# Performance work log

Hardware: AMD Instinct MI355X
Metric: run time of the kernel (lower is better)

The kernel has to match this reference:

```python
import jax, jax.numpy as jnp
import numpy as np

B, S, D, H, KD, VD, HID, L, V, OUTN = 16, 512, 512, 8, 64, 64, 2048, 4, 32000, 128
EPS = 1e-5


def _layer_norm(x, g, b):
    m = jnp.mean(x, axis=-1, keepdims=True)
    v = jnp.mean(jnp.square(x - m), axis=-1, keepdims=True)
    return (x - m) * jax.lax.rsqrt(v + EPS) * g + b


def _pos_encoding(seq_len, d_model):
    pos = jnp.arange(seq_len, dtype=jnp.float32)[:, None]
    div = jnp.exp(jnp.arange(0, d_model, 2, dtype=jnp.float32) * (-np.log(10000.0) / d_model))
    pe = jnp.zeros((seq_len, d_model), dtype=jnp.float32)
    pe = pe.at[:, 0::2].set(jnp.sin(pos * div))
    pe = pe.at[:, 1::2].set(jnp.cos(pos * div))
    return pe


def setup_inputs() -> dict:
    key = jax.random.key(0)
    ks = jax.random.split(key, 32)
    s = 0.02
    n = jax.random.normal
    inp = {
        "enc_inputs": jax.random.randint(ks[0], (B, S), 0, V, dtype=jnp.int32),
        "emb": n(ks[1], (V, D), jnp.float32) * s,
        # stacked per-layer params, leading dim = L
        "Wq": n(ks[2], (L, D, H * KD), jnp.float32) * s,
        "bq": jnp.zeros((L, H * KD), jnp.float32),
        "Wk": n(ks[3], (L, D, H * KD), jnp.float32) * s,
        "bk": jnp.zeros((L, H * KD), jnp.float32),
        "Wv": n(ks[4], (L, D, H * VD), jnp.float32) * s,
        "bv": jnp.zeros((L, H * VD), jnp.float32),
        "Wo": n(ks[5], (L, H * VD, D), jnp.float32) * s,
        "bo": jnp.zeros((L, D), jnp.float32),
        "ln1_g": jnp.ones((L, D), jnp.float32),
        "ln1_b": jnp.zeros((L, D), jnp.float32),
        "W1": n(ks[6], (L, D, HID), jnp.float32) * s,   # conv1d k=1 == linear
        "b1": jnp.zeros((L, HID), jnp.float32),
        "W2": n(ks[7], (L, HID, D), jnp.float32) * s,
        "b2": jnp.zeros((L, D), jnp.float32),
        "ln2_g": jnp.ones((L, D), jnp.float32),
        "ln2_b": jnp.zeros((L, D), jnp.float32),
        # flatten head created inside torch forward: [S*D, 128]
        "Wf": n(ks[8], (S * D, OUTN), jnp.float32) * s,
        "bf": jnp.zeros((OUTN,), jnp.float32),
        "Wout": n(ks[9], (OUTN, 1), jnp.float32) * s,
        "bout": jnp.zeros((1,), jnp.float32),
    }
    return inp


def _encoder(enc_inputs, emb, Wq, bq, Wk, bk, Wv, bv, Wo, bo, ln1_g, ln1_b,
             W1, b1, W2, b2, ln2_g, ln2_b, Wf, bf, Wout, bout):
    x = emb[enc_inputs] + _pos_encoding(S, D)[None, :, :]          # [B,S,D]
    pad = (enc_inputs == 0)[:, None, None, :]                      # [B,1,1,S]
    scale = 1.0 / np.sqrt(D)                                       # note: sqrt(embed_dim), as in source
    for l in range(L):
        # multi-head attention
        q = (x @ Wq[l] + bq[l]).reshape(B, S, H, KD)
        k = (x @ Wk[l] + bk[l]).reshape(B, S, H, KD)
        v = (x @ Wv[l] + bv[l]).reshape(B, S, H, VD)
        scores = jnp.einsum('bqhd,bkhd->bhqk', q, k) * scale
        scores = jnp.where(pad, -1e9, scores)
        attn = jax.nn.softmax(scores, axis=-1)
        ctx = jnp.einsum('bhqk,bkhd->bqhd', attn, v).reshape(B, S, H * VD)
        x = _layer_norm(ctx @ Wo[l] + bo[l] + x, ln1_g[l], ln1_b[l])
        # position-wise FFN (conv1d kernel_size=1)
        h = jax.nn.relu(x @ W1[l] + b1[l])
        x = _layer_norm(h @ W2[l] + b2[l] + x, ln2_g[l], ln2_b[l])
    flat = x.reshape(B, S * D)
    features = flat @ Wf + bf                                      # [B,128]
    y_score = jax.nn.sigmoid(features @ Wout + bout)               # [B,1]
    y_pred = jnp.round(y_score)
    return y_score, y_pred, features


def reference(enc_inputs, emb, Wq, bq, Wk, bk, Wv, bv, Wo, bo, ln1_g, ln1_b,
              W1, b1, W2, b2, ln2_g, ln2_b, Wf, bf, Wout, bout):
    return _encoder(enc_inputs, emb, Wq, bq, Wk, bk, Wv, bv, Wo, bo, ln1_g, ln1_b,
                    W1, b1, W2, b2, ln2_g, ln2_b, Wf, bf, Wout, bout)
```

## Files before the change

### kernel.cpp

```cpp
#include <hip/hip_runtime.h>
#include <hip/hip_bf16.h>
#include <math.h>

typedef unsigned short ushort_t;
typedef __attribute__((ext_vector_type(8))) short bf16x8;
typedef __attribute__((ext_vector_type(4))) float f32x4;

#define SCALE_QK 0.04419417382415922f
#define PE_C 0.017988946039015986f

__device__ __forceinline__ void g2lds16(const void* g, void* l) {
    __builtin_amdgcn_global_load_lds(
        (const __attribute__((address_space(1))) unsigned int*)g,
        (__attribute__((address_space(3))) unsigned int*)l,
        16, 0, 0);
}
__device__ __forceinline__ ushort_t f2bs(float v) {
    __hip_bfloat16 h = __float2bfloat16(v);
    return *reinterpret_cast<ushort_t*>(&h);
}
__device__ __forceinline__ float bs2f(ushort_t v) {
    return __uint_as_float(((unsigned int)v) << 16);
}

template<int BM, int BN, bool RELU, bool VT, bool STATS>
__global__ __launch_bounds__(256) void gemm2(
    const ushort_t* __restrict__ A, const ushort_t* __restrict__ B,
    const float* __restrict__ bias, const ushort_t* __restrict__ resb,
    ushort_t* __restrict__ C, float2* __restrict__ part,
    ushort_t* __restrict__ vt, int K, int lda, int ldb, int ldc)
{
    constexpr int MI = BM / 32, NJ = BN / 32;
    __shared__ ushort_t As[BM * 64];
    __shared__ ushort_t Bs[BN * 64];

    const int t = threadIdx.x;
    const int lane = t & 63, w = t >> 6;
    const int l16 = lane & 15, quad = lane >> 4;
    const int r8 = lane >> 3;
    const int kg = ((lane & 7) ^ r8) << 3;
    const int wm = (w >> 1) * (BM / 2);
    const int wn = (w & 1) * (BN / 2);

    const int m0 = blockIdx.y * BM, n0 = blockIdx.x * BN;

    f32x4 acc[MI][NJ];
    #pragma unroll
    for (int i = 0; i < MI; i++)
        #pragma unroll
        for (int j = 0; j < NJ; j++)
            acc[i][j] = (f32x4){0.f, 0.f, 0.f, 0.f};

    for (int k0 = 0; k0 < K; k0 += 64) {
        #pragma unroll
        for (int ii = 0; ii < BM / 32; ii++) {
            int rbase = w * (BM / 4) + ii * 8;
            g2lds16(A + (size_t)(m0 + rbase + r8) * lda + k0 + kg, &As[rbase * 64]);
        }
        #pragma unroll
        for (int ii = 0; ii < BN / 32; ii++) {
            int rbase = w * (BN / 4) + ii * 8;
            g2lds16(B + (size_t)(n0 + rbase + r8) * ldb + k0 + kg, &Bs[rbase * 64]);
        }
        __syncthreads();

        #pragma unroll
        for (int tt = 0; tt < 2; tt++) {
            bf16x8 af[MI], bf[NJ];
            #pragma unroll
            for (int i = 0; i < MI; i++) {
                int row = wm + i * 16 + l16;
                af[i] = *(const bf16x8*)&As[row * 64 + ((((tt << 2) + quad) ^ (row & 7)) << 3)];
            }
            #pragma unroll
            for (int j = 0; j < NJ; j++) {
                int row = wn + j * 16 + l16;
                bf[j] = *(const bf16x8*)&Bs[row * 64 + ((((tt << 2) + quad) ^ (row & 7)) << 3)];
            }
            #pragma unroll
            for (int i = 0; i < MI; i++)
                #pragma unroll
                for (int j = 0; j < NJ; j++)
                    acc[i][j] = __builtin_amdgcn_mfma_f32_16x16x32_bf16(
                        af[i], bf[j], acc[i][j], 0, 0, 0);
        }
        __syncthreads();
    }

    if (VT && n0 >= 1024) {
        #pragma unroll
        for (int i = 0; i < MI; i++) {
            int mbase = m0 + wm + i * 16 + quad * 4;
            int b = mbase >> 9, s = mbase & 511;
            #pragma unroll
            for (int j = 0; j < NJ; j++) {
                int n = n0 + wn + j * 16 + l16;
                int hv = n - 1024;
                int h = hv >> 6, vd = hv & 63;
                float bv = bias[n];
                ushort4 pk;
                pk.x = f2bs(acc[i][j][0] + bv);
                pk.y = f2bs(acc[i][j][1] + bv);
                pk.z = f2bs(acc[i][j][2] + bv);
                pk.w = f2bs(acc[i][j][3] + bv);
                *(ushort4*)&vt[((size_t)((b << 3) + h)) * 32768 + (size_t)vd * 512 + s] = pk;
            }
        }
        return;
    }

    #pragma unroll
    for (int i = 0; i < MI; i++) {
        float rs[4] = {0.f, 0.f, 0.f, 0.f}, rq[4] = {0.f, 0.f, 0.f, 0.f};
        #pragma unroll
        for (int j = 0; j < NJ; j++) {
            int n = n0 + wn + j * 16 + l16;
            float bv = bias ? bias[n] : 0.f;
            #pragma unroll
            for (int r = 0; r < 4; r++) {
                int m = m0 + wm + i * 16 + quad * 4 + r;
                float v = acc[i][j][r] + bv;
                if (resb) v += bs2f(resb[(size_t)m * ldc + n]);
                if (RELU) v = fmaxf(v, 0.f);
                C[(size_t)m * ldc + n] = f2bs(v);
                if (STATS) { rs[r] += v; rq[r] += v * v; }
            }
        }
        if (STATS) {
            #pragma unroll
            for (int r = 0; r < 4; r++) {
                float s = rs[r], q = rq[r];
                #pragma unroll
                for (int off = 1; off < 16; off <<= 1) {
                    s += __shfl_xor(s, off);
                    q += __shfl_xor(q, off);
                }
                if (l16 == 0) {
                    int m = m0 + wm + i * 16 + quad * 4 + r;
                    part[(size_t)m * 16 + blockIdx.x * 2 + (w & 1)] = make_float2(s, q);
                }
            }
        }
    }
}

template<bool RELU, bool VT>
__global__ __launch_bounds__(512, 2) void gemm8(
    const ushort_t* __restrict__ A, const ushort_t* __restrict__ B,
    const float* __restrict__ bias, ushort_t* __restrict__ C,
    ushort_t* __restrict__ vt, int K, int lda, int ldb, int ldc)
{
    __shared__ ushort_t As[2][256 * 64];
    __shared__ ushort_t Bs[2][256 * 64];

    const int t = threadIdx.x;
    const int lane = t & 63, w = t >> 6;
    const int l16 = lane & 15, quad = lane >> 4;
    const int r8 = lane >> 3;
    const int kg = ((lane & 7) ^ r8) << 3;
    const int wm = (w >> 2) * 128;
    const int wn = (w & 3) * 64;
    const int m0 = blockIdx.y * 256, n0 = blockIdx.x * 256;
    const int NT = K >> 6;

    f32x4 acc[8][4];
    #pragma unroll
    for (int i = 0; i < 8; i++)
        #pragma unroll
        for (int j = 0; j < 4; j++)
            acc[i][j] = (f32x4){0.f, 0.f, 0.f, 0.f};

    auto STAGE8 = [&](int kt, int bb) {
        int k0 = kt << 6;
        #pragma unroll
        for (int ii = 0; ii < 4; ii++) {
            int rbase = w * 32 + ii * 8;
            g2lds16(A + (size_t)(m0 + rbase + r8) * lda + k0 + kg,
                    &As[bb][rbase * 64]);
            g2lds16(B + (size_t)(n0 + rbase + r8) * ldb + k0 + kg,
                    &Bs[bb][rbase * 64]);
        }
    };

    STAGE8(0, 0);
    STAGE8(1, 1);

    for (int kt = 0; kt < NT; kt++) {
        const int bb = kt & 1;
        if (kt < NT - 1)
            asm volatile("s_waitcnt vmcnt(8)" ::: "memory");
        else
            asm volatile("s_waitcnt vmcnt(0)" ::: "memory");
        __builtin_amdgcn_s_barrier();
        asm volatile("" ::: "memory");

        #pragma unroll
        for (int tt = 0; tt < 2; tt++) {
            bf16x8 af[8], bf[4];
            #pragma unroll
            for (int i = 0; i < 8; i++) {
                int row = wm + i * 16 + l16;
                af[i] = *(const bf16x8*)&As[bb][row * 64 + ((((tt << 2) + quad) ^ (row & 7)) << 3)];
            }
            #pragma unroll
            for (int j = 0; j < 4; j++) {
                int row = wn + j * 16 + l16;
                bf[j] = *(const bf16x8*)&Bs[bb][row * 64 + ((((tt << 2) + quad) ^ (row & 7)) << 3)];
            }
            #pragma unroll
            for (int i = 0; i < 8; i++)
                #pragma unroll
                for (int j = 0; j < 4; j++)
                    acc[i][j] = __builtin_amdgcn_mfma_f32_16x16x32_bf16(
                        af[i], bf[j], acc[i][j], 0, 0, 0);
        }

        asm volatile("" ::: "memory");
        __builtin_amdgcn_s_barrier();
        asm volatile("" ::: "memory");
        if (kt + 2 < NT)
            STAGE8(kt + 2, bb);
    }

    if (VT && n0 >= 1024) {
        #pragma unroll
        for (int i = 0; i < 8; i++) {
            int mbase = m0 + wm + i * 16 + quad * 4;
            int b = mbase >> 9, s = mbase & 511;
            #pragma unroll
            for (int j = 0; j < 4; j++) {
                int n = n0 + wn + j * 16 + l16;
                int hv = n - 1024;
                int h = hv >> 6, vd = hv & 63;
                float bv = bias[n];
                ushort4 pk;
                pk.x = f2bs(acc[i][j][0] + bv);
                pk.y = f2bs(acc[i][j][1] + bv);
                pk.z = f2bs(acc[i][j][2] + bv);
                pk.w = f2bs(acc[i][j][3] + bv);
                *(ushort4*)&vt[((size_t)((b << 3) + h)) * 32768 + (size_t)vd * 512 + s] = pk;
            }
        }
        return;
    }

    #pragma unroll
    for (int i = 0; i < 8; i++)
        #pragma unroll
        for (int j = 0; j < 4; j++) {
            int n = n0 + wn + j * 16 + l16;
            float bv = bias[n];
            #pragma unroll
            for (int r = 0; r < 4; r++) {
                int m = m0 + wm + i * 16 + quad * 4 + r;
                float v = acc[i][j][r] + bv;
                if (RELU) v = fmaxf(v, 0.f);
                C[(size_t)m * ldc + n] = f2bs(v);
            }
        }
}

__global__ __launch_bounds__(256) void flash_attn(
    ushort_t* __restrict__ QKV, const ushort_t* __restrict__ Vt,
    const int* __restrict__ tok)
{
    __shared__ ushort_t Qs[128 * 64];
    __shared__ ushort_t Ks[128 * 64];
    __shared__ ushort_t Vts[64 * 128];
    __shared__ ushort_t Ps[128 * 128];

    const int bh = blockIdx.y;
    const int b = bh >> 3, h = bh & 7;
    const int q0 = blockIdx.x * 128;
    const int t = threadIdx.x;
    const int lane = t & 63, w = t >> 6;
    const int l16 = lane & 15, quad = lane >> 4;
    const int wm = w * 32;
    const size_t rowbase = (size_t)b * 512;

    {
        int r8 = lane >> 3;
        int kg = (lane & 7) ^ r8;
        #pragma unroll
        for (int ii = 0; ii < 4; ii++) {
            int rb = w * 32 + ii * 8;
            g2lds16(QKV + (rowbase + q0 + rb + r8) * 1536 + h * 64 + kg * 8,
                    &Qs[rb * 64]);
        }
    }

    f32x4 accO[2][4];
    #pragma unroll
    for (int i = 0; i < 2; i++)
        #pragma unroll
        for (int jv = 0; jv < 4; jv++)
            accO[i][jv] = (f32x4){0.f, 0.f, 0.f, 0.f};
    float lrow[2][4];
    #pragma unroll
    for (int i = 0; i < 2; i++)
        #pragma unroll
        for (int r = 0; r < 4; r++) lrow[i][r] = 0.f;

    for (int kc = 0; kc < 4; kc++) {
        __syncthreads();
        {
            int r8 = lane >> 3;
            int kg = (lane & 7) ^ r8;
            #pragma unroll
            for (int ii = 0; ii < 4; ii++) {
                int rb = w * 32 + ii * 8;
                g2lds16(QKV + (rowbase + kc * 128 + rb + r8) * 1536 + 512 + h * 64 + kg * 8,
                        &Ks[rb * 64]);
            }
        }
        {
            int v4 = lane >> 4;
            #pragma unroll
            for (int ii = 0; ii < 4; ii++) {
                int vb = w * 16 + ii * 4;
                int vd = vb + v4;
                int kg = (lane & 15) ^ (vd & 15);
                g2lds16(Vt + (size_t)bh * 32768 + (size_t)vd * 512 + kc * 128 + kg * 8,
                        &Vts[vb * 128]);
            }
        }
        float maskv[8];
        #pragma unroll
        for (int j = 0; j < 8; j++)
            maskv[j] = (tok[b * 512 + kc * 128 + j * 16 + l16] == 0) ? -1e9f : 0.f;

        __syncthreads();

        f32x4 sacc[2][8];
        #pragma unroll
        for (int i = 0; i < 2; i++)
            #pragma unroll
            for (int j = 0; j < 8; j++)
                sacc[i][j] = (f32x4){0.f, 0.f, 0.f, 0.f};
        #pragma unroll
        for (int tt = 0; tt < 2; tt++) {
            bf16x8 aq[2], bk8[8];
            #pragma unroll
            for (int i = 0; i < 2; i++) {
                int row = wm + i * 16 + l16;
                aq[i] = *(const bf16x8*)&Qs[row * 64 + (((tt << 2) + quad) ^ (row & 7)) * 8];
            }
            #pragma unroll
            for (int j = 0; j < 8; j++) {
                int row = j * 16 + l16;
                bk8[j] = *(const bf16x8*)&Ks[row * 64 + (((tt << 2) + quad) ^ (row & 7)) * 8];
            }
            #pragma unroll
            for (int i = 0; i < 2; i++)
                #pragma unroll
                for (int j = 0; j < 8; j++)
                    sacc[i][j] = __builtin_amdgcn_mfma_f32_16x16x32_bf16(
                        aq[i], bk8[j], sacc[i][j], 0, 0, 0);
        }

        #pragma unroll
        for (int i = 0; i < 2; i++)
            #pragma unroll
            for (int j = 0; j < 8; j++)
                #pragma unroll
                for (int r = 0; r < 4; r++) {
                    float p = __expf(fmaf(sacc[i][j][r], SCALE_QK, maskv[j]));
                    sacc[i][j][r] = p;
                    lrow[i][r] += p;
                }

        #pragma unroll
        for (int i = 0; i < 2; i++)
            #pragma unroll
            for (int j = 0; j < 8; j++) {
                int col = j * 16 + l16;
                int colc = col >> 3, csub = col & 7;
                #pragma unroll
                for (int r = 0; r < 4; r++) {
                    int row = wm + i * 16 + quad * 4 + r;
                    Ps[row * 128 + ((colc ^ (row & 15)) << 3) + csub] = f2bs(sacc[i][j][r]);
                }
            }

        #pragma unroll
        for (int tt = 0; tt < 4; tt++) {
            bf16x8 ap[2], bv8[4];
            #pragma unroll
            for (int i = 0; i < 2; i++) {
                int row = wm + i * 16 + l16;
                ap[i] = *(const bf16x8*)&Ps[row * 128 + ((((tt << 2) + quad)) ^ (row & 15)) * 8];
            }
            #pragma unroll
            for (int jv = 0; jv < 4; jv++) {
                int vd = jv * 16 + l16;
                bv8[jv] = *(const bf16x8*)&Vts[vd * 128 + (((tt << 2) + quad) ^ (vd & 15)) * 8];
            }
            #pragma unroll
            for (int i = 0; i < 2; i++)
                #pragma unroll
                for (int jv = 0; jv < 4; jv++)
                    accO[i][jv] = __builtin_amdgcn_mfma_f32_16x16x32_bf16(
                        ap[i], bv8[jv], accO[i][jv], 0, 0, 0);
        }
    }

    #pragma unroll
    for (int i = 0; i < 2; i++)
        #pragma unroll
        for (int r = 0; r < 4; r++) {
            float s = lrow[i][r];
            #pragma unroll
            for (int off = 1; off < 16; off <<= 1)
                s += __shfl_xor(s, off);
            float inv = 1.f / s;
            int row = q0 + wm + i * 16 + quad * 4 + r;
            #pragma unroll
            for (int jv = 0; jv < 4; jv++) {
                int vd = jv * 16 + l16;
                QKV[(rowbase + row) * 1536 + h * 64 + vd] = f2bs(accO[i][jv][r] * inv);
            }
        }
}

__global__ __launch_bounds__(256) void transpose_cvt(
    const float* __restrict__ in, __hip_bfloat16* __restrict__ out,
    int R, int Cc, long long inz, long long outz)
{
    in  += blockIdx.z * inz;
    out += blockIdx.z * outz;
    __shared__ float tile[32][33];
    int c0 = blockIdx.x * 32, r0 = blockIdx.y * 32;
    int tx = threadIdx.x & 31, ty = threadIdx.x >> 5;
    #pragma unroll
    for (int i = 0; i < 4; i++)
        tile[ty + i * 8][tx] = in[(size_t)(r0 + ty + i * 8) * Cc + c0 + tx];
    __syncthreads();
    #pragma unroll
    for (int i = 0; i < 4; i++)
        out[(size_t)(c0 + ty + i * 8) * R + r0 + tx] =
            __float2bfloat16(tile[tx][ty + i * 8]);
}

__global__ __launch_bounds__(256) void concat_bias(const float* __restrict__ bq,
                                                   const float* __restrict__ bk,
                                                   const float* __restrict__ bv,
                                                   float* __restrict__ bqkv) {
    int idx = blockIdx.x * 256 + threadIdx.x;
    if (idx >= 4 * 1536) return;
    int l = idx / 1536, n = idx - l * 1536;
    float v = (n < 512) ? bq[l * 512 + n]
            : (n < 1024) ? bk[l * 512 + n - 512]
                         : bv[l * 512 + n - 1024];
    bqkv[idx] = v;
}

__global__ __launch_bounds__(256) void embed_pe_b(const int* __restrict__ tok,
                                                  const float* __restrict__ emb,
                                                  __hip_bfloat16* __restrict__ xb) {
    int idx = blockIdx.x * 256 + threadIdx.x;
    int d  = idx & 511;
    int bs = idx >> 9;
    int s  = bs & 511;
    int t  = tok[bs];
    float freq  = expf(-(float)(d & ~1) * PE_C);
    float angle = (float)s * freq;
    float pe    = (d & 1) ? cosf(angle) : sinf(angle);
    xb[idx] = __float2bfloat16(emb[(size_t)t * 512 + d] + pe);
}

__global__ __launch_bounds__(256) void ln_stats(const ushort_t* __restrict__ Cpre,
                                                const float2* __restrict__ part,
                                                const float* __restrict__ g,
                                                const float* __restrict__ b,
                                                ushort_t* __restrict__ Xb) {
    long long row = blockIdx.x;
    int t = threadIdx.x;
    float s = 0.f, q = 0.f;
    if (t < 16) {
        float2 p = part[row * 16 + t];
        s = p.x; q = p.y;
    }
    #pragma unroll
    for (int off = 1; off < 16; off <<= 1) {
        s += __shfl_xor(s, off);
        q += __shfl_xor(q, off);
    }
    __shared__ float mv[2];
    if (t == 0) {
        float mean = s * (1.f / 512.f);
        float var = q * (1.f / 512.f) - mean * mean;
        mv[0] = mean;
        mv[1] = rsqrtf(var + 1e-5f);
    }
    __syncthreads();
    float mean = mv[0], r = mv[1];
    int c = t * 2;
    ushort2 u = *(const ushort2*)&Cpre[row * 512 + c];
    ushort2 o;
    o.x = f2bs((bs2f(u.x) - mean) * r * g[c]     + b[c]);
    o.y = f2bs((bs2f(u.y) - mean) * r * g[c + 1] + b[c + 1]);
    *(ushort2*)&Xb[row * 512 + c] = o;
}

__global__ __launch_bounds__(256) void feat_partial(const ushort_t* __restrict__ Xb,
                                                    const float* __restrict__ Wf,
                                                    float* __restrict__ FbP) {
    int slice = blockIdx.x;
    int k0 = slice * 512;
    __shared__ float Xs[16][512];
    int t = threadIdx.x;
    for (int i = t; i < 2048; i += 256) {
        int b = i >> 7, c4 = (i & 127) * 4;
        ushort4 u = *(const ushort4*)&Xb[(size_t)b * 262144 + k0 + c4];
        Xs[b][c4 + 0] = bs2f(u.x);
        Xs[b][c4 + 1] = bs2f(u.y);
        Xs[b][c4 + 2] = bs2f(u.z);
        Xs[b][c4 + 3] = bs2f(u.w);
    }
    __syncthreads();
    int n4 = (t & 31) * 4;
    int kh = t >> 5;
    float4 acc[16];
    #pragma unroll
    for (int b = 0; b < 16; b++) acc[b] = (float4){0.f, 0.f, 0.f, 0.f};
    for (int kk4 = 0; kk4 < 16; kk4++) {
        int kb = kh * 64 + kk4 * 4;
        float4 w0 = *(const float4*)&Wf[(size_t)(k0 + kb + 0) * 128 + n4];
        float4 w1 = *(const float4*)&Wf[(size_t)(k0 + kb + 1) * 128 + n4];
        float4 w2 = *(const float4*)&Wf[(size_t)(k0 + kb + 2) * 128 + n4];
        float4 w3 = *(const float4*)&Wf[(size_t)(k0 + kb + 3) * 128 + n4];
        #pragma unroll
        for (int b = 0; b < 16; b++) {
            float4 xq = *(const float4*)&Xs[b][kb];
            acc[b].x += xq.x * w0.x + xq.y * w1.x + xq.z * w2.x + xq.w * w3.x;
            acc[b].y += xq.x * w0.y + xq.y * w1.y + xq.z * w2.y + xq.w * w3.y;
            acc[b].z += xq.x * w0.z + xq.y * w1.z + xq.z * w2.z + xq.w * w3.z;
            acc[b].w += xq.x * w0.w + xq.y * w1.w + xq.z * w2.w + xq.w * w3.w;
        }
    }
    float* dst = FbP + ((size_t)slice * 8 + kh) * 2048;
    #pragma unroll
    for (int b = 0; b < 16; b++)
        *(float4*)&dst[b * 128 + n4] = acc[b];
}

__global__ __launch_bounds__(256) void feat_reduce(const float* __restrict__ FbP,
                                                   float* __restrict__ Fb) {
    int idx = blockIdx.x * 256 + threadIdx.x;
    int j0 = blockIdx.y * 128;
    float s = 0.f;
    for (int j = 0; j < 128; j++) s += FbP[(size_t)(j0 + j) * 2048 + idx];
    atomicAdd(&Fb[idx], s);
}

__global__ __launch_bounds__(256) void head_kernel(const float* __restrict__ feat,
                                                   const float* __restrict__ bfv,
                                                   const float* __restrict__ Wo2,
                                                   const float* __restrict__ bo2,
                                                   float* __restrict__ out) {
    __shared__ float f[2048];
    int t = threadIdx.x;
    for (int i = t; i < 2048; i += 256) {
        float v = feat[i] + bfv[i & 127];
        f[i] = v;
        out[32 + i] = v;
    }
    __syncthreads();
    if (t < 16) {
        float zv = bo2[0];
        for (int n = 0; n < 128; n++) zv = fmaf(f[t * 128 + n], Wo2[n], zv);
        float ys = 1.f / (1.f + expf(-zv));
        out[t] = ys;
        out[16 + t] = rintf(ys);
    }
}

extern "C" void kernel_launch(void* const* d_in, const int* in_sizes, int n_in,
                              void* d_out, int out_size, void* d_ws, size_t ws_size,
                              hipStream_t stream) {
    const int*   enc  = (const int*)  d_in[0];
    const float* emb  = (const float*)d_in[1];
    const float* Wq   = (const float*)d_in[2];
    const float* bq   = (const float*)d_in[3];
    const float* Wk   = (const float*)d_in[4];
    const float* bk   = (const float*)d_in[5];
    const float* Wv   = (const float*)d_in[6];
    const float* bv   = (const float*)d_in[7];
    const float* Wo   = (const float*)d_in[8];
    const float* bo   = (const float*)d_in[9];
    const float* g1   = (const float*)d_in[10];
    const float* be1  = (const float*)d_in[11];
    const float* W1   = (const float*)d_in[12];
    const float* b1f  = (const float*)d_in[13];
    const float* W2   = (const float*)d_in[14];
    const float* b2f  = (const float*)d_in[15];
    const float* g2   = (const float*)d_in[16];
    const float* be2  = (const float*)d_in[17];
    const float* Wf   = (const float*)d_in[18];
    const float* bf   = (const float*)d_in[19];
    const float* Wout = (const float*)d_in[20];
    const float* bout = (const float*)d_in[21];
    float* out = (float*)d_out;

    char* ws = (char*)d_ws;
    ushort_t* Cpre = (ushort_t*) (ws + 0);
    ushort_t* Xb   = (ushort_t*) (ws + 16777216);
    ushort_t* QKV  = (ushort_t*) (ws + 25165824);
    ushort_t* Vt   = (ushort_t*) (ws + 50331648);
    ushort_t* S    = (ushort_t*) (ws + 58720256);
    ushort_t* WqkvT= (ushort_t*) (ws + 92274688);
    ushort_t* WoT  = (ushort_t*) (ws + 98566144);
    ushort_t* W1T  = (ushort_t*) (ws + 100663296);
    ushort_t* W2T  = (ushort_t*) (ws + 109051904);
    float*    bqkv = (float*)    (ws + 117440512);
    float*    Fb   = (float*)    (ws + 117465088);
    float2*   part = (float2*)   (ws + 117473280);
    float*    FbP  = (float*)    (ws + 25165824);

    typedef __hip_bfloat16 bf16;

    transpose_cvt<<<dim3(16, 16, 4), 256, 0, stream>>>(Wq, (bf16*)WqkvT,            512, 512,  262144, 786432);
    transpose_cvt<<<dim3(16, 16, 4), 256, 0, stream>>>(Wk, (bf16*)(WqkvT + 262144), 512, 512,  262144, 786432);
    transpose_cvt<<<dim3(16, 16, 4), 256, 0, stream>>>(Wv, (bf16*)(WqkvT + 524288), 512, 512,  262144, 786432);
    transpose_cvt<<<dim3(16, 16, 4), 256, 0, stream>>>(Wo, (bf16*)WoT,              512, 512,  262144, 262144);
    transpose_cvt<<<dim3(64, 16, 4), 256, 0, stream>>>(W1, (bf16*)W1T,              512, 2048, 1048576, 1048576);
    transpose_cvt<<<dim3(16, 64, 4), 256, 0, stream>>>(W2, (bf16*)W2T,              2048, 512, 1048576, 1048576);
    concat_bias<<<24, 256, 0, stream>>>(bq, bk, bv, bqkv);

    embed_pe_b<<<16384, 256, 0, stream>>>(enc, emb, (bf16*)Xb);

    for (int l = 0; l < 4; l++) {
        gemm8<false, true><<<dim3(6, 32), 512, 0, stream>>>(
            Xb, WqkvT + (size_t)l * 786432, bqkv + l * 1536,
            QKV, Vt, 512, 512, 512, 1536);

        flash_attn<<<dim3(4, 128), 256, 0, stream>>>(QKV, Vt, enc);

        gemm2<128, 64, false, false, true><<<dim3(8, 64), 256, 0, stream>>>(
            QKV, WoT + (size_t)l * 262144, bo + l * 512, Xb,
            Cpre, part, nullptr, 512, 1536, 512, 512);
        ln_stats<<<8192, 256, 0, stream>>>(Cpre, part, g1 + l * 512, be1 + l * 512, Xb);

        gemm8<true, false><<<dim3(8, 32), 512, 0, stream>>>(
            Xb, W1T + (size_t)l * 1048576, b1f + l * 2048,
            S, nullptr, 512, 512, 512, 2048);
        gemm2<128, 64, false, false, true><<<dim3(8, 64), 256, 0, stream>>>(
            S, W2T + (size_t)l * 1048576, b2f + l * 512, Xb,
            Cpre, part, nullptr, 2048, 2048, 2048, 512);
        ln_stats<<<8192, 256, 0, stream>>>(Cpre, part, g2 + l * 512, be2 + l * 512, Xb);
    }

    hipMemsetAsync(Fb, 0, 2048 * sizeof(float), stream);
    feat_partial<<<512, 256, 0, stream>>>(Xb, Wf, FbP);
    feat_reduce<<<dim3(8, 32), 256, 0, stream>>>(FbP, Fb);
    head_kernel<<<1, 256, 0, stream>>>(Fb, bf, Wout, bout, out);
}
```

Baseline: 1.057 ms.

## Fuse LayerNorm into full-row output GEMMs and merge prep and feature-reduce kernels

Replaces the Wo and W2 GEMM plus separate ln_stats pass with a gemmLN kernel in which each block computes a full 32x512 output row tile. Inside that kernel it adds bias and residual, computes the LayerNorm statistics and writes the normalized output directly, with double-buffered async loads. This removes the Cpre round trip and the partial-stats buffer. The various weight transpose, bias concat, Fb zeroing and embedding kernels are merged into a single prep launch, and the feature reduction now uses LDS plus global atomics instead of a separate reduce kernel. The trade-off is only 256 blocks, each loading the whole 512-row B tile per k step, which may hurt occupancy and L2 traffic. The in-place read of the residual from Xb while writing Xb relies on each block owning distinct rows.

```diff
diff --git a/kernel.cpp b/kernel.cpp
--- a/kernel.cpp
+++ b/kernel.cpp
@@ -21,127 +21,6 @@
 }
 __device__ __forceinline__ float bs2f(ushort_t v) {
     return __uint_as_float(((unsigned int)v) << 16);
-}
-
-template<int BM, int BN, bool RELU, bool VT, bool STATS>
-__global__ __launch_bounds__(256) void gemm2(
-    const ushort_t* __restrict__ A, const ushort_t* __restrict__ B,
-    const float* __restrict__ bias, const ushort_t* __restrict__ resb,
-    ushort_t* __restrict__ C, float2* __restrict__ part,
-    ushort_t* __restrict__ vt, int K, int lda, int ldb, int ldc)
-{
-    constexpr int MI = BM / 32, NJ = BN / 32;
-    __shared__ ushort_t As[BM * 64];
-    __shared__ ushort_t Bs[BN * 64];
-
-    const int t = threadIdx.x;
-    const int lane = t & 63, w = t >> 6;
-    const int l16 = lane & 15, quad = lane >> 4;
-    const int r8 = lane >> 3;
-    const int kg = ((lane & 7) ^ r8) << 3;
-    const int wm = (w >> 1) * (BM / 2);
-    const int wn = (w & 1) * (BN / 2);
-
-    const int m0 = blockIdx.y * BM, n0 = blockIdx.x * BN;
-
-    f32x4 acc[MI][NJ];
-    #pragma unroll
-    for (int i = 0; i < MI; i++)
-        #pragma unroll
-        for (int j = 0; j < NJ; j++)
-            acc[i][j] = (f32x4){0.f, 0.f, 0.f, 0.f};
-
-    for (int k0 = 0; k0 < K; k0 += 64) {
-        #pragma unroll
-        for (int ii = 0; ii < BM / 32; ii++) {
-            int rbase = w * (BM / 4) + ii * 8;
-            g2lds16(A + (size_t)(m0 + rbase + r8) * lda + k0 + kg, &As[rbase * 64]);
-        }
-        #pragma unroll
-        for (int ii = 0; ii < BN / 32; ii++) {
-            int rbase = w * (BN / 4) + ii * 8;
-            g2lds16(B + (size_t)(n0 + rbase + r8) * ldb + k0 + kg, &Bs[rbase * 64]);
-        }
-        __syncthreads();
-
-        #pragma unroll
-        for (int tt = 0; tt < 2; tt++) {
-            bf16x8 af[MI], bf[NJ];
-            #pragma unroll
-            for (int i = 0; i < MI; i++) {
-                int row = wm + i * 16 + l16;
-                af[i] = *(const bf16x8*)&As[row * 64 + ((((tt << 2) + quad) ^ (row & 7)) << 3)];
-            }
-            #pragma unroll
-            for (int j = 0; j < NJ; j++) {
-                int row = wn + j * 16 + l16;
-                bf[j] = *(const bf16x8*)&Bs[row * 64 + ((((tt << 2) + quad) ^ (row & 7)) << 3)];
-            }
-            #pragma unroll
-            for (int i = 0; i < MI; i++)
-                #pragma unroll
-                for (int j = 0; j < NJ; j++)
-                    acc[i][j] = __builtin_amdgcn_mfma_f32_16x16x32_bf16(
-                        af[i], bf[j], acc[i][j], 0, 0, 0);
-        }
-        __syncthreads();
-    }
-
-    if (VT && n0 >= 1024) {
-        #pragma unroll
-        for (int i = 0; i < MI; i++) {
-            int mbase = m0 + wm + i * 16 + quad * 4;
-            int b = mbase >> 9, s = mbase & 511;
-            #pragma unroll
-            for (int j = 0; j < NJ; j++) {
-                int n = n0 + wn + j * 16 + l16;
-                int hv = n - 1024;
-                int h = hv >> 6, vd = hv & 63;
-                float bv = bias[n];
-                ushort4 pk;
-                pk.x = f2bs(acc[i][j][0] + bv);
-                pk.y = f2bs(acc[i][j][1] + bv);
-                pk.z = f2bs(acc[i][j][2] + bv);
-                pk.w = f2bs(acc[i][j][3] + bv);
-                *(ushort4*)&vt[((size_t)((b << 3) + h)) * 32768 + (size_t)vd * 512 + s] = pk;
-            }
-        }
-        return;
-    }
-
-    #pragma unroll
-    for (int i = 0; i < MI; i++) {
-        float rs[4] = {0.f, 0.f, 0.f, 0.f}, rq[4] = {0.f, 0.f, 0.f, 0.f};
-        #pragma unroll
-        for (int j = 0; j < NJ; j++) {
-            int n = n0 + wn + j * 16 + l16;
-            float bv = bias ? bias[n] : 0.f;
-            #pragma unroll
-            for (int r = 0; r < 4; r++) {
-                int m = m0 + wm + i * 16 + quad * 4 + r;
-                float v = acc[i][j][r] + bv;
-                if (resb) v += bs2f(resb[(size_t)m * ldc + n]);
-                if (RELU) v = fmaxf(v, 0.f);
-                C[(size_t)m * ldc + n] = f2bs(v);
-                if (STATS) { rs[r] += v; rq[r] += v * v; }
-            }
-        }
-        if (STATS) {
-            #pragma unroll
-            for (int r = 0; r < 4; r++) {
-                float s = rs[r], q = rq[r];
-                #pragma unroll
-                for (int off = 1; off < 16; off <<= 1) {
-                    s += __shfl_xor(s, off);
-                    q += __shfl_xor(q, off);
-                }
-                if (l16 == 0) {
-                    int m = m0 + wm + i * 16 + quad * 4 + r;
-                    part[(size_t)m * 16 + blockIdx.x * 2 + (w & 1)] = make_float2(s, q);
-                }
-            }
-        }
-    }
 }
 
 template<bool RELU, bool VT>
@@ -260,6 +139,150 @@
         }
 }
 
+__global__ __launch_bounds__(256) void gemmLN(
+    const ushort_t* __restrict__ A, const ushort_t* __restrict__ B,
+    const float* __restrict__ bias, const ushort_t* __restrict__ res,
+    const float* __restrict__ g, const float* __restrict__ bt,
+    ushort_t* __restrict__ X, int K, int lda)
+{
+    __shared__ ushort_t As[2][32 * 64];
+    __shared__ ushort_t Bs[2][512 * 64];
+    __shared__ float2 pst[4][32];
+    __shared__ float2 rmv[32];
+
+    const int t = threadIdx.x;
+    const int lane = t & 63, w = t >> 6;
+    const int l16 = lane & 15, quad = lane >> 4;
+    const int r8 = lane >> 3;
+    const int kg = ((lane & 7) ^ r8) << 3;
+    const int wn = w * 128;
+    const int m0 = blockIdx.x * 32;
+    const int NT = K >> 6;
+
+    f32x4 acc[2][8];
+    #pragma unroll
+    for (int i = 0; i < 2; i++)
+        #pragma unroll
+        for (int j = 0; j < 8; j++)
+            acc[i][j] = (f32x4){0.f, 0.f, 0.f, 0.f};
+
+    auto STAGE = [&](int kt, int bb) {
+        int k0 = kt << 6;
+        g2lds16(A + (size_t)(m0 + w * 8 + r8) * lda + k0 + kg,
+                &As[bb][(w * 8) * 64]);
+        #pragma unroll
+        for (int ii = 0; ii < 16; ii++) {
+            int rbase = w * 128 + ii * 8;
+            g2lds16(B + (size_t)(rbase + r8) * K + k0 + kg,
+                    &Bs[bb][rbase * 64]);
+        }
+    };
+
+    STAGE(0, 0);
+    STAGE(1, 1);
+
+    for (int kt = 0; kt < NT; kt++) {
+        const int bb = kt & 1;
+        if (kt < NT - 1)
+            asm volatile("s_waitcnt vmcnt(17)" ::: "memory");
+        else
+            asm volatile("s_waitcnt vmcnt(0)" ::: "memory");
+        __builtin_amdgcn_s_barrier();
+        asm volatile("" ::: "memory");
+
+        #pragma unroll
+        for (int tt = 0; tt < 2; tt++) {
+            bf16x8 af[2], bf8[8];
+            #pragma unroll
+            for (int i = 0; i < 2; i++) {
+                int row = i * 16 + l16;
+                af[i] = *(const bf16x8*)&As[bb][row * 64 + ((((tt << 2) + quad) ^ (row & 7)) << 3)];
+            }
+            #pragma unroll
+            for (int j = 0; j < 8; j++) {
+                int row = wn + j * 16 + l16;
+                bf8[j] = *(const bf16x8*)&Bs[bb][row * 64 + ((((tt << 2) + quad) ^ (row & 7)) << 3)];
+            }
+            #pragma unroll
+            for (int i = 0; i < 2; i++)
+                #pragma unroll
+                for (int j = 0; j < 8; j++)
+                    acc[i][j] = __builtin_amdgcn_mfma_f32_16x16x32_bf16(
+                        af[i], bf8[j], acc[i][j], 0, 0, 0);
+        }
+
+        asm volatile("" ::: "memory");
+        __builtin_amdgcn_s_barrier();
+        asm volatile("" ::: "memory");
+        if (kt + 2 < NT)
+            STAGE(kt + 2, bb);
+    }
+
+    float rs[2][4], rq[2][4];
+    #pragma unroll
+    for (int i = 0; i < 2; i++)
+        #pragma unroll
+        for (int r = 0; r < 4; r++) { rs[i][r] = 0.f; rq[i][r] = 0.f; }
+
+    #pragma unroll
+    for (int i = 0; i < 2; i++)
+        #pragma unroll
+        for (int j = 0; j < 8; j++) {
+            int n = wn + j * 16 + l16;
+            float bvn = bias[n];
+            #pragma unroll
+            for (int r = 0; r < 4; r++) {
+                int row = i * 16 + quad * 4 + r;
+                float v = acc[i][j][r] + bvn
+                        + bs2f(res[(size_t)(m0 + row) * 512 + n]);
+                acc[i][j][r] = v;
+                rs[i][r] += v;
+                rq[i][r] += v * v;
+            }
+        }
+
+    #pragma unroll
+    for (int i = 0; i < 2; i++)
+        #pragma unroll
+        for (int r = 0; r < 4; r++) {
+            #pragma unroll
+            for (int off = 1; off < 16; off <<= 1) {
+                rs[i][r] += __shfl_xor(rs[i][r], off);
+                rq[i][r] += __shfl_xor(rq[i][r], off);
+            }
+            if (l16 == 0)
+                pst[w][i * 16 + quad * 4 + r] = make_float2(rs[i][r], rq[i][r]);
+        }
+    __syncthreads();
+    if (t < 32) {
+        float s = 0.f, q = 0.f;
+        #pragma unroll
+        for (int wv = 0; wv < 4; wv++) {
+            float2 p = pst[wv][t];
+            s += p.x; q += p.y;
+        }
+        float mean = s * (1.f / 512.f);
+        float var = q * (1.f / 512.f) - mean * mean;
+        rmv[t] = make_float2(mean, rsqrtf(var + 1e-5f));
+    }
+    __syncthreads();
+
+    #pragma unroll
+    for (int i = 0; i < 2; i++)
+        #pragma unroll
+        for (int j = 0; j < 8; j++) {
+            int n = wn + j * 16 + l16;
+            float gn = g[n], btn = bt[n];
+            #pragma unroll
+            for (int r = 0; r < 4; r++) {
+                int row = i * 16 + quad * 4 + r;
+                float2 mr = rmv[row];
+                float o = (acc[i][j][r] - mr.x) * mr.y * gn + btn;
+                X[(size_t)(m0 + row) * 512 + n] = f2bs(o);
+            }
+        }
+}
+
 __global__ __launch_bounds__(256) void flash_attn(
     ushort_t* __restrict__ QKV, const ushort_t* __restrict__ Vt,
     const int* __restrict__ tok)
@@ -422,92 +445,84 @@
         }
 }
 
-__global__ __launch_bounds__(256) void transpose_cvt(
-    const float* __restrict__ in, __hip_bfloat16* __restrict__ out,
-    int R, int Cc, long long inz, long long outz)
+__global__ __launch_bounds__(256) void prep(
+    const float* __restrict__ Wq, const float* __restrict__ Wk,
+    const float* __restrict__ Wv, const float* __restrict__ Wo,
+    const float* __restrict__ W1, const float* __restrict__ W2,
+    const float* __restrict__ bq, const float* __restrict__ bk,
+    const float* __restrict__ bv, const int* __restrict__ tok,
+    const float* __restrict__ emb,
+    __hip_bfloat16* __restrict__ WqkvT, __hip_bfloat16* __restrict__ WoT,
+    __hip_bfloat16* __restrict__ W1T, __hip_bfloat16* __restrict__ W2T,
+    float* __restrict__ bqkv, float* __restrict__ Fb,
+    __hip_bfloat16* __restrict__ xb)
 {
-    in  += blockIdx.z * inz;
-    out += blockIdx.z * outz;
-    __shared__ float tile[32][33];
-    int c0 = blockIdx.x * 32, r0 = blockIdx.y * 32;
-    int tx = threadIdx.x & 31, ty = threadIdx.x >> 5;
-    #pragma unroll
-    for (int i = 0; i < 4; i++)
-        tile[ty + i * 8][tx] = in[(size_t)(r0 + ty + i * 8) * Cc + c0 + tx];
-    __syncthreads();
-    #pragma unroll
-    for (int i = 0; i < 4; i++)
-        out[(size_t)(c0 + ty + i * 8) * R + r0 + tx] =
-            __float2bfloat16(tile[tx][ty + i * 8]);
-}
-
-__global__ __launch_bounds__(256) void concat_bias(const float* __restrict__ bq,
-                                                   const float* __restrict__ bk,
-                                                   const float* __restrict__ bv,
-                                                   float* __restrict__ bqkv) {
-    int idx = blockIdx.x * 256 + threadIdx.x;
-    if (idx >= 4 * 1536) return;
-    int l = idx / 1536, n = idx - l * 1536;
-    float v = (n < 512) ? bq[l * 512 + n]
-            : (n < 1024) ? bk[l * 512 + n - 512]
-                         : bv[l * 512 + n - 1024];
-    bqkv[idx] = v;
-}
-
-__global__ __launch_bounds__(256) void embed_pe_b(const int* __restrict__ tok,
-                                                  const float* __restrict__ emb,
-                                                  __hip_bfloat16* __restrict__ xb) {
-    int idx = blockIdx.x * 256 + threadIdx.x;
-    int d  = idx & 511;
-    int bs = idx >> 9;
-    int s  = bs & 511;
-    int t  = tok[bs];
-    float freq  = expf(-(float)(d & ~1) * PE_C);
-    float angle = (float)s * freq;
-    float pe    = (d & 1) ? cosf(angle) : sinf(angle);
-    xb[idx] = __float2bfloat16(emb[(size_t)t * 512 + d] + pe);
-}
-
-__global__ __launch_bounds__(256) void ln_stats(const ushort_t* __restrict__ Cpre,
-                                                const float2* __restrict__ part,
-                                                const float* __restrict__ g,
-                                                const float* __restrict__ b,
-                                                ushort_t* __restrict__ Xb) {
-    long long row = blockIdx.x;
-    int t = threadIdx.x;
-    float s = 0.f, q = 0.f;
-    if (t < 16) {
-        float2 p = part[row * 16 + t];
-        s = p.x; q = p.y;
-    }
-    #pragma unroll
-    for (int off = 1; off < 16; off <<= 1) {
-        s += __shfl_xor(s, off);
-        q += __shfl_xor(q, off);
-    }
-    __shared__ float mv[2];
-    if (t == 0) {
-        float mean = s * (1.f / 512.f);
-        float var = q * (1.f / 512.f) - mean * mean;
-        mv[0] = mean;
-        mv[1] = rsqrtf(var + 1e-5f);
-    }
-    __syncthreads();
-    float mean = mv[0], r = mv[1];
-    int c = t * 2;
-    ushort2 u = *(const ushort2*)&Cpre[row * 512 + c];
-    ushort2 o;
-    o.x = f2bs((bs2f(u.x) - mean) * r * g[c]     + b[c]);
-    o.y = f2bs((bs2f(u.y) - mean) * r * g[c + 1] + b[c + 1]);
-    *(ushort2*)&Xb[row * 512 + c] = o;
+    const int blk = blockIdx.x;
+    const int t = threadIdx.x;
+
+    if (blk < 12288) {
+        __shared__ float tile[32][33];
+        const float* in; __hip_bfloat16* out;
+        long long inz, outz; int R, Cc, bx, by, bz;
+        if (blk < 4096) {
+            int seg = blk >> 10, lb = blk & 1023;
+            bz = lb >> 8; by = (lb >> 4) & 15; bx = lb & 15;
+            R = 512; Cc = 512; inz = 262144;
+            if      (seg == 0) { in = Wq; out = WqkvT;          outz = 786432; }
+            else if (seg == 1) { in = Wk; out = WqkvT + 262144; outz = 786432; }
+            else if (seg == 2) { in = Wv; out = WqkvT + 524288; outz = 786432; }
+            else               { in = Wo; out = WoT;            outz = 262144; }
+        } else if (blk < 8192) {
+            int lb = blk - 4096;
+            bz = lb >> 10; by = (lb >> 6) & 15; bx = lb & 63;
+            R = 512; Cc = 2048; inz = 1048576; outz = 1048576;
+            in = W1; out = W1T;
+        } else {
+            int lb = blk - 8192;
+            bz = lb >> 10; by = (lb >> 4) & 63; bx = lb & 15;
+            R = 2048; Cc = 512; inz = 1048576; outz = 1048576;
+            in = W2; out = W2T;
+        }
+        in += bz * inz; out += bz * outz;
+        int c0 = bx * 32, r0 = by * 32;
+        int tx = t & 31, ty = t >> 5;
+        #pragma unroll
+        for (int i = 0; i < 4; i++)
+            tile[ty + i * 8][tx] = in[(size_t)(r0 + ty + i * 8) * Cc + c0 + tx];
+        __syncthreads();
+        #pragma unroll
+        for (int i = 0; i < 4; i++)
+            out[(size_t)(c0 + ty + i * 8) * R + r0 + tx] =
+                __float2bfloat16(tile[tx][ty + i * 8]);
+    } else if (blk < 12312) {
+        int k = blk - 12288;
+        int idx = k * 256 + t;
+        int l = idx / 1536, n = idx - l * 1536;
+        float v = (n < 512) ? bq[l * 512 + n]
+                : (n < 1024) ? bk[l * 512 + n - 512]
+                             : bv[l * 512 + n - 1024];
+        bqkv[idx] = v;
+        if (k < 8) Fb[k * 256 + t] = 0.f;
+    } else {
+        int idx = (blk - 12312) * 256 + t;
+        int d  = idx & 511;
+        int bs = idx >> 9;
+        int s  = bs & 511;
+        int tk = tok[bs];
+        float freq  = expf(-(float)(d & ~1) * PE_C);
+        float angle = (float)s * freq;
+        float pe    = (d & 1) ? cosf(angle) : sinf(angle);
+        xb[idx] = __float2bfloat16(emb[(size_t)tk * 512 + d] + pe);
+    }
 }
 
 __global__ __launch_bounds__(256) void feat_partial(const ushort_t* __restrict__ Xb,
                                                     const float* __restrict__ Wf,
-                                                    float* __restrict__ FbP) {
+                                                    float* __restrict__ Fb) {
     int slice = blockIdx.x;
     int k0 = slice * 512;
     __shared__ float Xs[16][512];
+    __shared__ float Red[2048];
     int t = threadIdx.x;
     for (int i = t; i < 2048; i += 256) {
         int b = i >> 7, c4 = (i & 127) * 4;
@@ -516,6 +531,7 @@
         Xs[b][c4 + 1] = bs2f(u.y);
         Xs[b][c4 + 2] = bs2f(u.z);
         Xs[b][c4 + 3] = bs2f(u.w);
+        Red[i] = 0.f;
     }
     __syncthreads();
     int n4 = (t & 31) * 4;
@@ -538,19 +554,16 @@
             acc[b].w += xq.x * w0.w + xq.y * w1.w + xq.z * w2.w + xq.w * w3.w;
         }
     }
-    float* dst = FbP + ((size_t)slice * 8 + kh) * 2048;
-    #pragma unroll
-    for (int b = 0; b < 16; b++)
-        *(float4*)&dst[b * 128 + n4] = acc[b];
-}
-
-__global__ __launch_bounds__(256) void feat_reduce(const float* __restrict__ FbP,
-                                                   float* __restrict__ Fb) {
-    int idx = blockIdx.x * 256 + threadIdx.x;
-    int j0 = blockIdx.y * 128;
-    float s = 0.f;
-    for (int j = 0; j < 128; j++) s += FbP[(size_t)(j0 + j) * 2048 + idx];
-    atomicAdd(&Fb[idx], s);
+    #pragma unroll
+    for (int b = 0; b < 16; b++) {
+        atomicAdd(&Red[b * 128 + n4 + 0], acc[b].x);
+        atomicAdd(&Red[b * 128 + n4 + 1], acc[b].y);
+        atomicAdd(&Red[b * 128 + n4 + 2], acc[b].z);
+        atomicAdd(&Red[b * 128 + n4 + 3], acc[b].w);
+    }
+    __syncthreads();
+    for (int o = t; o < 2048; o += 256)
+        atomicAdd(&Fb[o], Red[o]);
 }
 
 __global__ __launch_bounds__(256) void head_kernel(const float* __restrict__ feat,
@@ -603,7 +616,6 @@
     float* out = (float*)d_out;
 
     char* ws = (char*)d_ws;
-    ushort_t* Cpre = (ushort_t*) (ws + 0);
     ushort_t* Xb   = (ushort_t*) (ws + 16777216);
     ushort_t* QKV  = (ushort_t*) (ws + 25165824);
     ushort_t* Vt   = (ushort_t*) (ws + 50331648);
@@ -614,20 +626,12 @@
     ushort_t* W2T  = (ushort_t*) (ws + 109051904);
     float*    bqkv = (float*)    (ws + 117440512);
     float*    Fb   = (float*)    (ws + 117465088);
-    float2*   part = (float2*)   (ws + 117473280);
-    float*    FbP  = (float*)    (ws + 25165824);
 
     typedef __hip_bfloat16 bf16;
 
-    transpose_cvt<<<dim3(16, 16, 4), 256, 0, stream>>>(Wq, (bf16*)WqkvT,            512, 512,  262144, 786432);
-    transpose_cvt<<<dim3(16, 16, 4), 256, 0, stream>>>(Wk, (bf16*)(WqkvT + 262144), 512, 512,  262144, 786432);
-    transpose_cvt<<<dim3(16, 16, 4), 256, 0, stream>>>(Wv, (bf16*)(WqkvT + 524288), 512, 512,  262144, 786432);
-    transpose_cvt<<<dim3(16, 16, 4), 256, 0, stream>>>(Wo, (bf16*)WoT,              512, 512,  262144, 262144);
-    transpose_cvt<<<dim3(64, 16, 4), 256, 0, stream>>>(W1, (bf16*)W1T,              512, 2048, 1048576, 1048576);
-    transpose_cvt<<<dim3(16, 64, 4), 256, 0, stream>>>(W2, (bf16*)W2T,              2048, 512, 1048576, 1048576);
-    concat_bias<<<24, 256, 0, stream>>>(bq, bk, bv, bqkv);
-
-    embed_pe_b<<<16384, 256, 0, stream>>>(enc, emb, (bf16*)Xb);
+    prep<<<28696, 256, 0, stream>>>(
+        Wq, Wk, Wv, Wo, W1, W2, bq, bk, bv, enc, emb,
+        (bf16*)WqkvT, (bf16*)WoT, (bf16*)W1T, (bf16*)W2T, bqkv, Fb, (bf16*)Xb);
 
     for (int l = 0; l < 4; l++) {
         gemm8<false, true><<<dim3(6, 32), 512, 0, stream>>>(
@@ -636,22 +640,19 @@
 
         flash_attn<<<dim3(4, 128), 256, 0, stream>>>(QKV, Vt, enc);
 
-        gemm2<128, 64, false, false, true><<<dim3(8, 64), 256, 0, stream>>>(
+        gemmLN<<<256, 256, 0, stream>>>(
             QKV, WoT + (size_t)l * 262144, bo + l * 512, Xb,
-            Cpre, part, nullptr, 512, 1536, 512, 512);
-        ln_stats<<<8192, 256, 0, stream>>>(Cpre, part, g1 + l * 512, be1 + l * 512, Xb);
+            g1 + l * 512, be1 + l * 512, Xb, 512, 1536);
 
         gemm8<true, false><<<dim3(8, 32), 512, 0, stream>>>(
             Xb, W1T + (size_t)l * 1048576, b1f + l * 2048,
             S, nullptr, 512, 512, 512, 2048);
-        gemm2<128, 64, false, false, true><<<dim3(8, 64), 256, 0, stream>>>(
+
+        gemmLN<<<256, 256, 0, stream>>>(
             S, W2T + (size_t)l * 1048576, b2f + l * 512, Xb,
-            Cpre, part, nullptr, 2048, 2048, 2048, 512);
-        ln_stats<<<8192, 256, 0, stream>>>(Cpre, part, g2 + l * 512, be2 + l * 512, Xb);
-    }
-
-    hipMemsetAsync(Fb, 0, 2048 * sizeof(float), stream);
-    feat_partial<<<512, 256, 0, stream>>>(Xb, Wf, FbP);
-    feat_reduce<<<dim3(8, 32), 256, 0, stream>>>(FbP, Fb);
+            g2 + l * 512, be2 + l * 512, Xb, 2048, 2048);
+    }
+
+    feat_partial<<<512, 256, 0, stream>>>(Xb, Wf, Fb);
     head_kernel<<<1, 256, 0, stream>>>(Fb, bf, Wout, bout, out);
 }
```

Measured after the change: 987.9 us. 6.5% less time.
